# Performance work log

Measured on AMD Instinct MI355X. Metric: run time of the kernel, lower is better.

Reference implementation:

```python
import jax, jax.numpy as jnp
import numpy as np

N = 100000        # points
C_IN = 64         # in_planes
C_OUT = 64        # out_planes (== mid_planes)
SHARE = 8         # share_planes
NS = 16           # nsample
CW = C_OUT // SHARE  # attention channels (8)
EPS = 1e-5


def _bn(x, gamma, beta):
    # PointBatchNorm in training mode: normalize over all axes except channel (last)
    ax = tuple(range(x.ndim - 1))
    m = jnp.mean(x, axis=ax)
    v = jnp.var(x, axis=ax)
    return gamma * (x - m) * jax.lax.rsqrt(v + EPS) + beta


def setup_inputs() -> dict:
    key = jax.random.key(0)
    ks = jax.random.split(key, 20)
    s = 0.05
    inp = {
        "p": jax.random.normal(ks[0], (N, 3), jnp.float32) * 5.0,
        "x": jax.random.normal(ks[1], (N, C_IN), jnp.float32),
        "o": jnp.array([N], jnp.int32),
        "idx": jax.random.randint(ks[2], (N, NS), 0, N, jnp.int32),
        # q/k/v linears
        "Wq": jax.random.normal(ks[3], (C_IN, C_OUT), jnp.float32) * s,
        "bq": jnp.zeros((C_OUT,), jnp.float32),
        "Wk": jax.random.normal(ks[4], (C_IN, C_OUT), jnp.float32) * s,
        "bk": jnp.zeros((C_OUT,), jnp.float32),
        "Wv": jax.random.normal(ks[5], (C_IN, C_OUT), jnp.float32) * s,
        "bv": jnp.zeros((C_OUT,), jnp.float32),
        # linear_p: Linear(3,3) -> BN(3) -> ReLU -> Linear(3,out)
        "Wp1": jax.random.normal(ks[6], (3, 3), jnp.float32) * 0.5,
        "bp1": jnp.zeros((3,), jnp.float32),
        "gp": jnp.ones((3,), jnp.float32),
        "betap": jnp.zeros((3,), jnp.float32),
        "Wp2": jax.random.normal(ks[7], (3, C_OUT), jnp.float32) * s,
        "bp2": jnp.zeros((C_OUT,), jnp.float32),
        # linear_w: BN(mid)->ReLU->Linear(mid, CW)->BN(CW)->ReLU->Linear(CW, CW)
        "gw1": jnp.ones((C_OUT,), jnp.float32),
        "bw1": jnp.zeros((C_OUT,), jnp.float32),
        "Ww1": jax.random.normal(ks[8], (C_OUT, CW), jnp.float32) * s,
        "bww1": jnp.zeros((CW,), jnp.float32),
        "gw2": jnp.ones((CW,), jnp.float32),
        "bw2": jnp.zeros((CW,), jnp.float32),
        "Ww2": jax.random.normal(ks[9], (CW, CW), jnp.float32) * s,
        "bww2": jnp.zeros((CW,), jnp.float32),
    }
    return inp


def reference(p, x, o, idx,
              Wq, bq, Wk, bk, Wv, bv,
              Wp1, bp1, gp, betap, Wp2, bp2,
              gw1, bw1, Ww1, bww1, gw2, bw2, Ww2, bww2):
    relu = jax.nn.relu
    x_q = x @ Wq + bq                       # [n, mid]
    x_k = x @ Wk + bk                       # [n, mid]
    x_v = x @ Wv + bv                       # [n, out]
    # knn_query_and_group: gather neighbors (idx precomputed), with relative xyz
    p_r0 = p[idx] - p[:, None, :]           # [n, ns, 3]
    xk_g = x_k[idx]                         # [n, ns, mid]
    xv_g = x_v[idx]                         # [n, ns, out]
    # linear_p
    p_r = relu(_bn(p_r0 @ Wp1 + bp1, gp, betap)) @ Wp2 + bp2   # [n, ns, out]
    # einops.reduce 'n ns (i j) -> n ns j' with j=mid_planes: i==1 -> identity
    r_qk = xk_g - x_q[:, None, :] + p_r     # [n, ns, mid]
    # linear_w
    w = relu(_bn(r_qk, gw1, bw1)) @ Ww1 + bww1          # [n, ns, CW]
    w = relu(_bn(w, gw2, bw2)) @ Ww2 + bww2             # [n, ns, CW]
    w = jax.nn.softmax(w, axis=1)                        # softmax over neighbors
    # shared-channel weighted sum
    v = (xv_g + p_r).reshape(N, NS, SHARE, CW)           # [n, ns, s, i]
    out = jnp.einsum('ntsi,nti->nsi', v, w)              # [n, s, i]
    return out.reshape(N, C_OUT)
```

## Files before the change

kernel.cpp:

```cpp
#include <hip/hip_runtime.h>
#include <math.h>

#define NPTS 100000
#define NSAMP 16
#define NROWS (NPTS*NSAMP)
#define EPS 1e-5f

#define NQKV ((NPTS + 63)/64)
#define GRID_B 1024
#define GRID_C 2048
#define GRID_D 2048
#define GRID_E 2048

#define S_BN1A 0
#define S_BN1B 4
#define S_BN2A 8
#define S_BN2B 72
#define S_BN3A 136
#define S_BN3B 144
#define S_PARTB 160
#define S_PARTC (S_PARTB + GRID_B*8)
#define S_PARTD (S_PARTC + GRID_C*128)

typedef __attribute__((ext_vector_type(8))) _Float16 f16x8;
typedef __attribute__((ext_vector_type(4))) float f32x4;

__device__ __forceinline__ float bf2f(unsigned short u) {
    return __uint_as_float(((unsigned int)u) << 16);
}
__device__ __forceinline__ unsigned int cvt_pk_bf16(float lo, float hi) {
    unsigned int r;
    asm("v_cvt_pk_bf16_f32 %0, %1, %2" : "=v"(r) : "v"(lo), "v"(hi));
    return r;
}
__device__ __forceinline__ float rlF(float v, int t) {
    return __int_as_float(__builtin_amdgcn_readlane(__float_as_int(v), t));
}

__global__ __launch_bounds__(256) void qkv_bn1_kernel(
    const float* __restrict__ x,
    const float* __restrict__ Wq, const float* __restrict__ bq,
    const float* __restrict__ Wk, const float* __restrict__ bk,
    const float* __restrict__ Wv, const float* __restrict__ bv,
    float* __restrict__ xq, unsigned short* __restrict__ xkb,
    unsigned short* __restrict__ xvb,
    const float* __restrict__ p, const int* __restrict__ idx,
    const float* __restrict__ Wp1, const float* __restrict__ bp1,
    float* __restrict__ part)
{
    __shared__ __align__(16) float xsh[64][68];
    __shared__ __align__(16) float wsh[64][64];
    __shared__ float red16[4][6];
    const int tid = threadIdx.x;

    if (blockIdx.x >= NQKV) {
        const int b = blockIdx.x - NQKV;
        float w9[9], bb[3];
        #pragma unroll
        for (int i = 0; i < 9; ++i) w9[i] = Wp1[i];
        #pragma unroll
        for (int i = 0; i < 3; ++i) bb[i] = bp1[i];

        float s0=0.f,s1=0.f,s2=0.f,q0=0.f,q1=0.f,q2=0.f;
        for (int row = b*256 + tid; row < NROWS; row += GRID_B*256) {
            const int n = row >> 4;
            const int j = idx[row];
            const float d0 = p[j*3+0] - p[n*3+0];
            const float d1 = p[j*3+1] - p[n*3+1];
            const float d2 = p[j*3+2] - p[n*3+2];
            const float t0 = d0*w9[0] + d1*w9[3] + d2*w9[6] + bb[0];
            const float t1 = d0*w9[1] + d1*w9[4] + d2*w9[7] + bb[1];
            const float t2 = d0*w9[2] + d1*w9[5] + d2*w9[8] + bb[2];
            s0 += t0; s1 += t1; s2 += t2;
            q0 += t0*t0; q1 += t1*t1; q2 += t2*t2;
        }
        #pragma unroll
        for (int m = 32; m >= 1; m >>= 1) {
            s0 += __shfl_xor(s0, m); s1 += __shfl_xor(s1, m); s2 += __shfl_xor(s2, m);
            q0 += __shfl_xor(q0, m); q1 += __shfl_xor(q1, m); q2 += __shfl_xor(q2, m);
        }
        const int lane = tid & 63, wid = tid >> 6;
        if (lane == 0) {
            red16[wid][0]=s0; red16[wid][1]=s1; red16[wid][2]=s2;
            red16[wid][3]=q0; red16[wid][4]=q1; red16[wid][5]=q2;
        }
        __syncthreads();
        if (tid < 6)
            part[b*8 + tid] = red16[0][tid]+red16[1][tid]+red16[2][tid]+red16[3][tid];
        return;
    }

    const int r0 = blockIdx.x * 64;
    {
        const int row = tid >> 4, c4 = tid & 15;
        #pragma unroll
        for (int rr = 0; rr < 4; ++rr) {
            const int r = row + rr*16;
            const int gr = r0 + r;
            float4 v = (gr < NPTS) ? *(const float4*)&x[(size_t)gr*64 + c4*4]
                                   : make_float4(0.f, 0.f, 0.f, 0.f);
            *(float4*)&xsh[r][c4*4] = v;
        }
    }

    const int tr = tid >> 4, tc = tid & 15;

    for (int m = 0; m < 3; ++m) {
        const float* __restrict__ W  = (m == 0) ? Wq : (m == 1) ? Wk : Wv;
        const float* __restrict__ bs = (m == 0) ? bq : (m == 1) ? bk : bv;

        __syncthreads();
        for (int l = tid; l < 1024; l += 256)
            *(float4*)&wsh[l >> 4][(l & 15)*4] = *(const float4*)&W[l*4];
        __syncthreads();

        float acc[4][4];
        {
            const float4 b4 = *(const float4*)&bs[tc*4];
            #pragma unroll
            for (int rr = 0; rr < 4; ++rr) {
                acc[rr][0] = b4.x; acc[rr][1] = b4.y;
                acc[rr][2] = b4.z; acc[rr][3] = b4.w;
            }
        }

        #pragma unroll 4
        for (int k4 = 0; k4 < 16; ++k4) {
            float4 xr[4];
            #pragma unroll
            for (int rr = 0; rr < 4; ++rr)
                xr[rr] = *(const float4*)&xsh[tr + 16*rr][k4*4];
            float4 wr[4];
            #pragma unroll
            for (int kk = 0; kk < 4; ++kk)
                wr[kk] = *(const float4*)&wsh[k4*4 + kk][tc*4];
            #pragma unroll
            for (int rr = 0; rr < 4; ++rr) {
                acc[rr][0] += xr[rr].x*wr[0].x + xr[rr].y*wr[1].x + xr[rr].z*wr[2].x + xr[rr].w*wr[3].x;
                acc[rr][1] += xr[rr].x*wr[0].y + xr[rr].y*wr[1].y + xr[rr].z*wr[2].y + xr[rr].w*wr[3].y;
                acc[rr][2] += xr[rr].x*wr[0].z + xr[rr].y*wr[1].z + xr[rr].z*wr[2].z + xr[rr].w*wr[3].z;
                acc[rr][3] += xr[rr].x*wr[0].w + xr[rr].y*wr[1].w + xr[rr].z*wr[2].w + xr[rr].w*wr[3].w;
            }
        }

        #pragma unroll
        for (int rr = 0; rr < 4; ++rr) {
            const int gr = r0 + tr + 16*rr;
            if (gr < NPTS) {
                if (m == 0) {
                    float4 o;
                    o.x = acc[rr][0]; o.y = acc[rr][1]; o.z = acc[rr][2]; o.w = acc[rr][3];
                    *(float4*)&xq[(size_t)gr*64 + tc*4] = o;
                } else {
                    unsigned short* dst = (m == 1) ? xkb : xvb;
                    uint2 o;
                    o.x = cvt_pk_bf16(acc[rr][0], acc[rr][1]);
                    o.y = cvt_pk_bf16(acc[rr][2], acc[rr][3]);
                    *(uint2*)&dst[(size_t)gr*64 + tc*4] = o;
                }
            }
        }
    }
}

__global__ __launch_bounds__(256) void bn_fin_kernel(
    const float* __restrict__ part, int nblk, int stride, int nch,
    const float* __restrict__ g, const float* __restrict__ beta,
    float* __restrict__ aout, float* __restrict__ bout)
{
    const int c = blockIdx.x;
    const int tid = threadIdx.x;
    float s = 0.f, q = 0.f;
    for (int b = tid; b < nblk; b += 256) {
        s += part[(size_t)b*stride + c];
        q += part[(size_t)b*stride + nch + c];
    }
    #pragma unroll
    for (int m = 32; m >= 1; m >>= 1) { s += __shfl_xor(s, m); q += __shfl_xor(q, m); }
    __shared__ float rs[4], rq[4];
    if ((tid & 63) == 0) { rs[tid >> 6] = s; rq[tid >> 6] = q; }
    __syncthreads();
    if (tid == 0) {
        s = rs[0]+rs[1]+rs[2]+rs[3];
        q = rq[0]+rq[1]+rq[2]+rq[3];
        const float inv = 1.0f / (float)NROWS;
        const float mean = s * inv;
        const float var = fmaxf(q * inv - mean*mean, 0.f);
        const float a = g[c] * rsqrtf(var + EPS);
        aout[c] = a;
        bout[c] = beta[c] - a * mean;
    }
}

__global__ __launch_bounds__(256, 8) void bn2_stats_kernel(
    const float* __restrict__ p, const int* __restrict__ idx,
    const float* __restrict__ xq, const unsigned short* __restrict__ xkb,
    const float* __restrict__ Wp1, const float* __restrict__ bp1,
    const float* __restrict__ Wp2, const float* __restrict__ bp2,
    const float* __restrict__ st, float* __restrict__ part)
{
    const int tid = threadIdx.x, lane = tid & 63, wid = tid >> 6;
    float w9[9], bb[3], a1[3], b1[3];
    #pragma unroll
    for (int i = 0; i < 9; ++i) w9[i] = Wp1[i];
    #pragma unroll
    for (int i = 0; i < 3; ++i) { bb[i] = bp1[i]; a1[i] = st[S_BN1A+i]; b1[i] = st[S_BN1B+i]; }
    const float wc0 = Wp2[lane], wc1 = Wp2[64+lane], wc2 = Wp2[128+lane], bpc = bp2[lane];
    const int lane16 = lane & 15;

    float s = 0.f, q = 0.f;
    const int nw = gridDim.x * 4;
    for (int pt = blockIdx.x*4 + wid; pt < NPTS; pt += nw) {
        const float xqc = xq[(size_t)pt*64 + lane];
        const int jreg = idx[pt*16 + lane16];
        const float pn0 = p[pt*3], pn1 = p[pt*3+1], pn2 = p[pt*3+2];
        const float d0 = p[jreg*3] - pn0, d1 = p[jreg*3+1] - pn1, d2 = p[jreg*3+2] - pn2;
        const float t0 = d0*w9[0] + d1*w9[3] + d2*w9[6] + bb[0];
        const float t1 = d0*w9[1] + d1*w9[4] + d2*w9[7] + bb[1];
        const float t2 = d0*w9[2] + d1*w9[5] + d2*w9[8] + bb[2];
        const float h0 = fmaxf(a1[0]*t0 + b1[0], 0.f);
        const float h1 = fmaxf(a1[1]*t1 + b1[1], 0.f);
        const float h2 = fmaxf(a1[2]*t2 + b1[2], 0.f);

        #pragma unroll
        for (int t = 0; t < 16; ++t) {
            const int jt = __builtin_amdgcn_readlane(jreg, t);
            const float g0 = rlF(h0, t), g1 = rlF(h1, t), g2 = rlF(h2, t);
            const float pr = fmaf(g0, wc0, fmaf(g1, wc1, fmaf(g2, wc2, bpc)));
            const float r = bf2f(xkb[(size_t)jt*64 + lane]) - xqc + pr;
            s += r; q = fmaf(r, r, q);
        }
    }
    __shared__ float redS[4][64], redQ[4][64];
    redS[wid][lane] = s; redQ[wid][lane] = q;
    __syncthreads();
    if (tid < 64) {
        const float S = redS[0][tid]+redS[1][tid]+redS[2][tid]+redS[3][tid];
        const float Q = redQ[0][tid]+redQ[1][tid]+redQ[2][tid]+redQ[3][tid];
        part[(size_t)blockIdx.x*128 + tid] = S;
        part[(size_t)blockIdx.x*128 + 64 + tid] = Q;
    }
}

__global__ __launch_bounds__(256, 8) void w1_kernel(
    const float* __restrict__ p, const int* __restrict__ idx,
    const float* __restrict__ xq, const unsigned short* __restrict__ xkb,
    const float* __restrict__ Wp1, const float* __restrict__ bp1,
    const float* __restrict__ Wp2, const float* __restrict__ bp2,
    const float* __restrict__ Ww1, const float* __restrict__ bww1,
    const float* __restrict__ st, unsigned short* __restrict__ w1out,
    float* __restrict__ part)
{
    __shared__ __align__(16) _Float16 hl[4][16][64];
    const int tid = threadIdx.x, lane = tid & 63, wid = tid >> 6;

    float w9[9], bb[3], a1[3], b1[3];
    #pragma unroll
    for (int i = 0; i < 9; ++i) w9[i] = Wp1[i];
    #pragma unroll
    for (int i = 0; i < 3; ++i) { bb[i] = bp1[i]; a1[i] = st[S_BN1A+i]; b1[i] = st[S_BN1B+i]; }

    const int c = lane;
    const float wc0 = Wp2[c], wc1 = Wp2[64+c], wc2 = Wp2[128+c], bpc = bp2[c];
    const float a2c = st[S_BN2A + c], b2c = st[S_BN2B + c];
    const int lane16 = lane & 15;
    const int kgrp = lane >> 4;

    f16x8 aF0, aF1;
    {
        const int m = lane16;
        #pragma unroll
        for (int i = 0; i < 8; ++i) {
            const int k0 = kgrp*4 + (i & 3) + 16*(i >> 2);
            const int i0 = (m < 8) ? (k0*8 + m) : 0;
            const int i1 = (m < 8) ? ((k0 + 32)*8 + m) : 0;
            aF0[i] = (m < 8) ? (_Float16)Ww1[i0] : (_Float16)0.f;
            aF1[i] = (m < 8) ? (_Float16)Ww1[i1] : (_Float16)0.f;
        }
    }
    f32x4 cb;
    #pragma unroll
    for (int r = 0; r < 4; ++r) cb[r] = bww1[(kgrp*4 + r) & 7];

    float s3[4] = {0.f,0.f,0.f,0.f}, q3[4] = {0.f,0.f,0.f,0.f};
    const int nw = gridDim.x * 4;
    for (int pt = blockIdx.x*4 + wid; pt < NPTS; pt += nw) {
        const float xqc = xq[(size_t)pt*64 + lane];
        const int jreg = idx[pt*16 + lane16];
        const float pn0 = p[pt*3], pn1 = p[pt*3+1], pn2 = p[pt*3+2];
        const float d0 = p[jreg*3] - pn0, d1 = p[jreg*3+1] - pn1, d2 = p[jreg*3+2] - pn2;
        const float t0v = d0*w9[0] + d1*w9[3] + d2*w9[6] + bb[0];
        const float t1v = d0*w9[1] + d1*w9[4] + d2*w9[7] + bb[1];
        const float t2v = d0*w9[2] + d1*w9[5] + d2*w9[8] + bb[2];
        const float h0 = fmaxf(a1[0]*t0v + b1[0], 0.f);
        const float h1 = fmaxf(a1[1]*t1v + b1[1], 0.f);
        const float h2 = fmaxf(a1[2]*t2v + b1[2], 0.f);

        #pragma unroll
        for (int t = 0; t < 16; ++t) {
            const int jt = __builtin_amdgcn_readlane(jreg, t);
            const float g0 = rlF(h0, t), g1 = rlF(h1, t), g2 = rlF(h2, t);
            const float pr = fmaf(g0, wc0, fmaf(g1, wc1, fmaf(g2, wc2, bpc)));
            const float r = bf2f(xkb[(size_t)jt*64 + lane]) - xqc + pr;
            hl[wid][t][lane ^ ((t & 7) << 3)] = (_Float16)fmaxf(fmaf(a2c, r, b2c), 0.f);
        }

        const int t = lane16;
        const int key = (t & 7) << 3;
        union { f16x8 v; uint2 u[2]; } b0u, b1u;
        b0u.u[0] = *(const uint2*)&hl[wid][t][(kgrp*4)      ^ key];
        b0u.u[1] = *(const uint2*)&hl[wid][t][(kgrp*4 + 16) ^ key];
        b1u.u[0] = *(const uint2*)&hl[wid][t][(kgrp*4 + 32) ^ key];
        b1u.u[1] = *(const uint2*)&hl[wid][t][(kgrp*4 + 48) ^ key];

        f32x4 acc = __builtin_amdgcn_mfma_f32_16x16x32_f16(aF0, b0u.v, cb, 0, 0, 0);
        acc = __builtin_amdgcn_mfma_f32_16x16x32_f16(aF1, b1u.v, acc, 0, 0, 0);

        if (lane < 32) {
            uint2 o;
            o.x = cvt_pk_bf16(acc[0], acc[1]);
            o.y = cvt_pk_bf16(acc[2], acc[3]);
            *(uint2*)&w1out[(size_t)pt*128 + lane16*8 + kgrp*4] = o;
            #pragma unroll
            for (int r = 0; r < 4; ++r) {
                s3[r] += acc[r];
                q3[r] = fmaf(acc[r], acc[r], q3[r]);
            }
        }
    }

    #pragma unroll
    for (int m = 8; m >= 1; m >>= 1) {
        #pragma unroll
        for (int r = 0; r < 4; ++r) {
            s3[r] += __shfl_xor(s3[r], m);
            q3[r] += __shfl_xor(q3[r], m);
        }
    }
    __shared__ float redS[4][8], redQ[4][8];
    if (lane == 0 || lane == 16) {
        const int jb = (lane >> 4) * 4;
        #pragma unroll
        for (int r = 0; r < 4; ++r) { redS[wid][jb+r] = s3[r]; redQ[wid][jb+r] = q3[r]; }
    }
    __syncthreads();
    if (tid < 8) {
        const float S = redS[0][tid]+redS[1][tid]+redS[2][tid]+redS[3][tid];
        const float Q = redQ[0][tid]+redQ[1][tid]+redQ[2][tid]+redQ[3][tid];
        part[(size_t)blockIdx.x*16 + tid]     = S;
        part[(size_t)blockIdx.x*16 + 8 + tid] = Q;
    }
}

__global__ __launch_bounds__(256, 8) void out_kernel(
    const float* __restrict__ p, const int* __restrict__ idx,
    const unsigned short* __restrict__ xvb, const unsigned short* __restrict__ w1b,
    const float* __restrict__ Wp1, const float* __restrict__ bp1,
    const float* __restrict__ Wp2, const float* __restrict__ bp2,
    const float* __restrict__ Ww2, const float* __restrict__ bww2,
    const float* __restrict__ st, float* __restrict__ out)
{
    __shared__ float wl[4][16][8];
    const int tid = threadIdx.x, lane = tid & 63, wid = tid >> 6;
    const int j8 = lane & 7, t0 = lane >> 3;
    const int lane16 = lane & 15;

    float w9[9], bb[3], a1[3], b1[3];
    #pragma unroll
    for (int i = 0; i < 9; ++i) w9[i] = Wp1[i];
    #pragma unroll
    for (int i = 0; i < 3; ++i) { bb[i] = bp1[i]; a1[i] = st[S_BN1A+i]; b1[i] = st[S_BN1B+i]; }
    float ww2c[8];
    #pragma unroll
    for (int i = 0; i < 8; ++i) ww2c[i] = Ww2[i*8 + j8];
    const float a3j = st[S_BN3A + j8], b3j = st[S_BN3B + j8];
    const float bw2j = bww2[j8];
    const int c = lane;
    const float wc0 = Wp2[c], wc1 = Wp2[64+c], wc2 = Wp2[128+c], bpc = bp2[c];

    const int nw = gridDim.x * 4;
    for (int pt = blockIdx.x*4 + wid; pt < NPTS; pt += nw) {
        const int jreg = idx[pt*16 + lane16];
        const float pn0 = p[pt*3], pn1 = p[pt*3+1], pn2 = p[pt*3+2];
        const float d0 = p[jreg*3] - pn0, d1 = p[jreg*3+1] - pn1, d2 = p[jreg*3+2] - pn2;
        const float t1v = d0*w9[0] + d1*w9[3] + d2*w9[6] + bb[0];
        const float t2v = d0*w9[1] + d1*w9[4] + d2*w9[7] + bb[1];
        const float t3v = d0*w9[2] + d1*w9[5] + d2*w9[8] + bb[2];
        const float h0 = fmaxf(a1[0]*t1v + b1[0], 0.f);
        const float h1 = fmaxf(a1[1]*t2v + b1[1], 0.f);
        const float h2 = fmaxf(a1[2]*t3v + b1[2], 0.f);

        const float val0 = bf2f(w1b[(size_t)pt*128 + lane]);
        const float val1 = bf2f(w1b[(size_t)pt*128 + 64 + lane]);
        const float r0 = fmaxf(a3j*val0 + b3j, 0.f);
        const float r1 = fmaxf(a3j*val1 + b3j, 0.f);
        float v0 = bw2j, v1 = bw2j;
        const int gbase = lane & 56;
        #pragma unroll
        for (int jj = 0; jj < 8; ++jj) {
            v0 += __shfl(r0, gbase + jj) * ww2c[jj];
            v1 += __shfl(r1, gbase + jj) * ww2c[jj];
        }
        float e0 = __expf(v0), e1 = __expf(v1);
        float ssum = e0 + e1;
        ssum += __shfl_xor(ssum, 8);
        ssum += __shfl_xor(ssum, 16);
        ssum += __shfl_xor(ssum, 32);
        const float inv = 1.0f / ssum;
        wl[wid][t0][j8]     = e0 * inv;
        wl[wid][t0 + 8][j8] = e1 * inv;

        float acc = 0.f;
        #pragma unroll
        for (int t = 0; t < 16; ++t) {
            const int jt = __builtin_amdgcn_readlane(jreg, t);
            const float g0 = rlF(h0, t), g1 = rlF(h1, t), g2 = rlF(h2, t);
            const float pr = fmaf(g0, wc0, fmaf(g1, wc1, fmaf(g2, wc2, bpc)));
            const float wt = wl[wid][t][j8];
            acc = fmaf(bf2f(xvb[(size_t)jt*64 + c]) + pr, wt, acc);
        }
        out[(size_t)pt*64 + c] = acc;
    }
}

extern "C" void kernel_launch(void* const* d_in, const int* in_sizes, int n_in,
                              void* d_out, int out_size, void* d_ws, size_t ws_size,
                              hipStream_t stream)
{
    const float* p    = (const float*)d_in[0];
    const float* x    = (const float*)d_in[1];
    const int*   idx  = (const int*)d_in[3];
    const float* Wq   = (const float*)d_in[4];
    const float* bq   = (const float*)d_in[5];
    const float* Wk   = (const float*)d_in[6];
    const float* bk   = (const float*)d_in[7];
    const float* Wv   = (const float*)d_in[8];
    const float* bv   = (const float*)d_in[9];
    const float* Wp1  = (const float*)d_in[10];
    const float* bp1  = (const float*)d_in[11];
    const float* gp   = (const float*)d_in[12];
    const float* betap= (const float*)d_in[13];
    const float* Wp2  = (const float*)d_in[14];
    const float* bp2  = (const float*)d_in[15];
    const float* gw1  = (const float*)d_in[16];
    const float* bw1  = (const float*)d_in[17];
    const float* Ww1  = (const float*)d_in[18];
    const float* bww1 = (const float*)d_in[19];
    const float* gw2  = (const float*)d_in[20];
    const float* bw2  = (const float*)d_in[21];
    const float* Ww2  = (const float*)d_in[22];
    const float* bww2 = (const float*)d_in[23];

    float* out = (float*)d_out;
    float* ws  = (float*)d_ws;

    float*          xq  = ws;
    unsigned short* xkb = (unsigned short*)(ws + (size_t)NPTS*64);
    unsigned short* xvb = (unsigned short*)(ws + (size_t)NPTS*96);
    unsigned short* w1b = (unsigned short*)(ws + (size_t)NPTS*128);
    float*          st  = ws + (size_t)NPTS*192;

    qkv_bn1_kernel<<<NQKV + GRID_B, 256, 0, stream>>>(
        x, Wq, bq, Wk, bk, Wv, bv, xq, xkb, xvb,
        p, idx, Wp1, bp1, st + S_PARTB);
    bn_fin_kernel<<<3, 256, 0, stream>>>(st + S_PARTB, GRID_B, 8, 3, gp, betap,
                                         st + S_BN1A, st + S_BN1B);

    bn2_stats_kernel<<<GRID_C, 256, 0, stream>>>(p, idx, xq, xkb, Wp1, bp1, Wp2, bp2,
                                                 st, st + S_PARTC);
    bn_fin_kernel<<<64, 256, 0, stream>>>(st + S_PARTC, GRID_C, 128, 64, gw1, bw1,
                                          st + S_BN2A, st + S_BN2B);

    w1_kernel<<<GRID_D, 256, 0, stream>>>(p, idx, xq, xkb, Wp1, bp1, Wp2, bp2,
                                          Ww1, bww1, st, w1b, st + S_PARTD);
    bn_fin_kernel<<<8, 256, 0, stream>>>(st + S_PARTD, GRID_D, 16, 8, gw2, bw2,
                                         st + S_BN3A, st + S_BN3B);

    out_kernel<<<GRID_E, 256, 0, stream>>>(p, idx, xvb, w1b, Wp1, bp1, Wp2, bp2,
                                           Ww2, bww2, st, out);
}
```

Measured before the change: 252.8 us.

## Cache linear_p first-layer outputs in bf16 and store xq as bf16

The first pass now writes the pre-BN linear_p outputs (t0..t2) per neighbor row as packed bf16. The three later kernels read these instead of re-gathering p at random neighbor indices and recomputing the 3x3 linear. xq is also stored in bf16 rather than fp32, halving its traffic. This trades three random gathers of p per row for one coalesced 8-byte load, at the cost of an extra 12.8 MB write and bf16 rounding of both xq and the pre-BN positional features.

```diff
diff --git a/kernel.cpp b/kernel.cpp
--- a/kernel.cpp
+++ b/kernel.cpp
@@ -42,11 +42,11 @@
     const float* __restrict__ Wq, const float* __restrict__ bq,
     const float* __restrict__ Wk, const float* __restrict__ bk,
     const float* __restrict__ Wv, const float* __restrict__ bv,
-    float* __restrict__ xq, unsigned short* __restrict__ xkb,
+    unsigned short* __restrict__ xqb, unsigned short* __restrict__ xkb,
     unsigned short* __restrict__ xvb,
     const float* __restrict__ p, const int* __restrict__ idx,
     const float* __restrict__ Wp1, const float* __restrict__ bp1,
-    float* __restrict__ part)
+    unsigned short* __restrict__ tb, float* __restrict__ part)
 {
     __shared__ __align__(16) float xsh[64][68];
     __shared__ __align__(16) float wsh[64][64];
@@ -71,6 +71,10 @@
             const float t0 = d0*w9[0] + d1*w9[3] + d2*w9[6] + bb[0];
             const float t1 = d0*w9[1] + d1*w9[4] + d2*w9[7] + bb[1];
             const float t2 = d0*w9[2] + d1*w9[5] + d2*w9[8] + bb[2];
+            uint2 o;
+            o.x = cvt_pk_bf16(t0, t1);
+            o.y = cvt_pk_bf16(t2, 0.f);
+            *(uint2*)&tb[(size_t)row*4] = o;
             s0 += t0; s1 += t1; s2 += t2;
             q0 += t0*t0; q1 += t1*t1; q2 += t2*t2;
         }
@@ -108,6 +112,7 @@
     for (int m = 0; m < 3; ++m) {
         const float* __restrict__ W  = (m == 0) ? Wq : (m == 1) ? Wk : Wv;
         const float* __restrict__ bs = (m == 0) ? bq : (m == 1) ? bk : bv;
+        unsigned short* __restrict__ dst = (m == 0) ? xqb : (m == 1) ? xkb : xvb;
 
         __syncthreads();
         for (int l = tid; l < 1024; l += 256)
@@ -147,17 +152,10 @@
         for (int rr = 0; rr < 4; ++rr) {
             const int gr = r0 + tr + 16*rr;
             if (gr < NPTS) {
-                if (m == 0) {
-                    float4 o;
-                    o.x = acc[rr][0]; o.y = acc[rr][1]; o.z = acc[rr][2]; o.w = acc[rr][3];
-                    *(float4*)&xq[(size_t)gr*64 + tc*4] = o;
-                } else {
-                    unsigned short* dst = (m == 1) ? xkb : xvb;
-                    uint2 o;
-                    o.x = cvt_pk_bf16(acc[rr][0], acc[rr][1]);
-                    o.y = cvt_pk_bf16(acc[rr][2], acc[rr][3]);
-                    *(uint2*)&dst[(size_t)gr*64 + tc*4] = o;
-                }
+                uint2 o;
+                o.x = cvt_pk_bf16(acc[rr][0], acc[rr][1]);
+                o.y = cvt_pk_bf16(acc[rr][2], acc[rr][3]);
+                *(uint2*)&dst[(size_t)gr*64 + tc*4] = o;
             }
         }
     }
@@ -193,31 +191,27 @@
 }
 
 __global__ __launch_bounds__(256, 8) void bn2_stats_kernel(
-    const float* __restrict__ p, const int* __restrict__ idx,
-    const float* __restrict__ xq, const unsigned short* __restrict__ xkb,
-    const float* __restrict__ Wp1, const float* __restrict__ bp1,
+    const int* __restrict__ idx, const unsigned short* __restrict__ tb,
+    const unsigned short* __restrict__ xqb, const unsigned short* __restrict__ xkb,
     const float* __restrict__ Wp2, const float* __restrict__ bp2,
     const float* __restrict__ st, float* __restrict__ part)
 {
     const int tid = threadIdx.x, lane = tid & 63, wid = tid >> 6;
-    float w9[9], bb[3], a1[3], b1[3];
-    #pragma unroll
-    for (int i = 0; i < 9; ++i) w9[i] = Wp1[i];
-    #pragma unroll
-    for (int i = 0; i < 3; ++i) { bb[i] = bp1[i]; a1[i] = st[S_BN1A+i]; b1[i] = st[S_BN1B+i]; }
+    float a1[3], b1[3];
+    #pragma unroll
+    for (int i = 0; i < 3; ++i) { a1[i] = st[S_BN1A+i]; b1[i] = st[S_BN1B+i]; }
     const float wc0 = Wp2[lane], wc1 = Wp2[64+lane], wc2 = Wp2[128+lane], bpc = bp2[lane];
     const int lane16 = lane & 15;
 
     float s = 0.f, q = 0.f;
     const int nw = gridDim.x * 4;
     for (int pt = blockIdx.x*4 + wid; pt < NPTS; pt += nw) {
-        const float xqc = xq[(size_t)pt*64 + lane];
+        const float xqc = bf2f(xqb[(size_t)pt*64 + lane]);
         const int jreg = idx[pt*16 + lane16];
-        const float pn0 = p[pt*3], pn1 = p[pt*3+1], pn2 = p[pt*3+2];
-        const float d0 = p[jreg*3] - pn0, d1 = p[jreg*3+1] - pn1, d2 = p[jreg*3+2] - pn2;
-        const float t0 = d0*w9[0] + d1*w9[3] + d2*w9[6] + bb[0];
-        const float t1 = d0*w9[1] + d1*w9[4] + d2*w9[7] + bb[1];
-        const float t2 = d0*w9[2] + d1*w9[5] + d2*w9[8] + bb[2];
+        const uint2 tv = *(const uint2*)&tb[(size_t)(pt*16 + lane16)*4];
+        const float t0 = bf2f((unsigned short)tv.x);
+        const float t1 = bf2f((unsigned short)(tv.x >> 16));
+        const float t2 = bf2f((unsigned short)tv.y);
         const float h0 = fmaxf(a1[0]*t0 + b1[0], 0.f);
         const float h1 = fmaxf(a1[1]*t1 + b1[1], 0.f);
         const float h2 = fmaxf(a1[2]*t2 + b1[2], 0.f);
@@ -243,9 +237,8 @@
 }
 
 __global__ __launch_bounds__(256, 8) void w1_kernel(
-    const float* __restrict__ p, const int* __restrict__ idx,
-    const float* __restrict__ xq, const unsigned short* __restrict__ xkb,
-    const float* __restrict__ Wp1, const float* __restrict__ bp1,
+    const int* __restrict__ idx, const unsigned short* __restrict__ tb,
+    const unsigned short* __restrict__ xqb, const unsigned short* __restrict__ xkb,
     const float* __restrict__ Wp2, const float* __restrict__ bp2,
     const float* __restrict__ Ww1, const float* __restrict__ bww1,
     const float* __restrict__ st, unsigned short* __restrict__ w1out,
@@ -254,11 +247,9 @@
     __shared__ __align__(16) _Float16 hl[4][16][64];
     const int tid = threadIdx.x, lane = tid & 63, wid = tid >> 6;
 
-    float w9[9], bb[3], a1[3], b1[3];
-    #pragma unroll
-    for (int i = 0; i < 9; ++i) w9[i] = Wp1[i];
-    #pragma unroll
-    for (int i = 0; i < 3; ++i) { bb[i] = bp1[i]; a1[i] = st[S_BN1A+i]; b1[i] = st[S_BN1B+i]; }
+    float a1[3], b1[3];
+    #pragma unroll
+    for (int i = 0; i < 3; ++i) { a1[i] = st[S_BN1A+i]; b1[i] = st[S_BN1B+i]; }
 
     const int c = lane;
     const float wc0 = Wp2[c], wc1 = Wp2[64+c], wc2 = Wp2[128+c], bpc = bp2[c];
@@ -285,13 +276,12 @@
     float s3[4] = {0.f,0.f,0.f,0.f}, q3[4] = {0.f,0.f,0.f,0.f};
     const int nw = gridDim.x * 4;
     for (int pt = blockIdx.x*4 + wid; pt < NPTS; pt += nw) {
-        const float xqc = xq[(size_t)pt*64 + lane];
+        const float xqc = bf2f(xqb[(size_t)pt*64 + lane]);
         const int jreg = idx[pt*16 + lane16];
-        const float pn0 = p[pt*3], pn1 = p[pt*3+1], pn2 = p[pt*3+2];
-        const float d0 = p[jreg*3] - pn0, d1 = p[jreg*3+1] - pn1, d2 = p[jreg*3+2] - pn2;
-        const float t0v = d0*w9[0] + d1*w9[3] + d2*w9[6] + bb[0];
-        const float t1v = d0*w9[1] + d1*w9[4] + d2*w9[7] + bb[1];
-        const float t2v = d0*w9[2] + d1*w9[5] + d2*w9[8] + bb[2];
+        const uint2 tv = *(const uint2*)&tb[(size_t)(pt*16 + lane16)*4];
+        const float t0v = bf2f((unsigned short)tv.x);
+        const float t1v = bf2f((unsigned short)(tv.x >> 16));
+        const float t2v = bf2f((unsigned short)tv.y);
         const float h0 = fmaxf(a1[0]*t0v + b1[0], 0.f);
         const float h1 = fmaxf(a1[1]*t1v + b1[1], 0.f);
         const float h2 = fmaxf(a1[2]*t2v + b1[2], 0.f);
@@ -353,9 +343,8 @@
 }
 
 __global__ __launch_bounds__(256, 8) void out_kernel(
-    const float* __restrict__ p, const int* __restrict__ idx,
+    const int* __restrict__ idx, const unsigned short* __restrict__ tb,
     const unsigned short* __restrict__ xvb, const unsigned short* __restrict__ w1b,
-    const float* __restrict__ Wp1, const float* __restrict__ bp1,
     const float* __restrict__ Wp2, const float* __restrict__ bp2,
     const float* __restrict__ Ww2, const float* __restrict__ bww2,
     const float* __restrict__ st, float* __restrict__ out)
@@ -365,11 +354,9 @@
     const int j8 = lane & 7, t0 = lane >> 3;
     const int lane16 = lane & 15;
 
-    float w9[9], bb[3], a1[3], b1[3];
-    #pragma unroll
-    for (int i = 0; i < 9; ++i) w9[i] = Wp1[i];
-    #pragma unroll
-    for (int i = 0; i < 3; ++i) { bb[i] = bp1[i]; a1[i] = st[S_BN1A+i]; b1[i] = st[S_BN1B+i]; }
+    float a1[3], b1[3];
+    #pragma unroll
+    for (int i = 0; i < 3; ++i) { a1[i] = st[S_BN1A+i]; b1[i] = st[S_BN1B+i]; }
     float ww2c[8];
     #pragma unroll
     for (int i = 0; i < 8; ++i) ww2c[i] = Ww2[i*8 + j8];
@@ -381,11 +368,10 @@
     const int nw = gridDim.x * 4;
     for (int pt = blockIdx.x*4 + wid; pt < NPTS; pt += nw) {
         const int jreg = idx[pt*16 + lane16];
-        const float pn0 = p[pt*3], pn1 = p[pt*3+1], pn2 = p[pt*3+2];
-        const float d0 = p[jreg*3] - pn0, d1 = p[jreg*3+1] - pn1, d2 = p[jreg*3+2] - pn2;
-        const float t1v = d0*w9[0] + d1*w9[3] + d2*w9[6] + bb[0];
-        const float t2v = d0*w9[1] + d1*w9[4] + d2*w9[7] + bb[1];
-        const float t3v = d0*w9[2] + d1*w9[5] + d2*w9[8] + bb[2];
+        const uint2 tv = *(const uint2*)&tb[(size_t)(pt*16 + lane16)*4];
+        const float t1v = bf2f((unsigned short)tv.x);
+        const float t2v = bf2f((unsigned short)(tv.x >> 16));
+        const float t3v = bf2f((unsigned short)tv.y);
         const float h0 = fmaxf(a1[0]*t1v + b1[0], 0.f);
         const float h1 = fmaxf(a1[1]*t2v + b1[1], 0.f);
         const float h2 = fmaxf(a1[2]*t3v + b1[2], 0.f);
@@ -454,28 +440,29 @@
     float* out = (float*)d_out;
     float* ws  = (float*)d_ws;
 
-    float*          xq  = ws;
-    unsigned short* xkb = (unsigned short*)(ws + (size_t)NPTS*64);
-    unsigned short* xvb = (unsigned short*)(ws + (size_t)NPTS*96);
-    unsigned short* w1b = (unsigned short*)(ws + (size_t)NPTS*128);
+    unsigned short* xqb = (unsigned short*)ws;
+    unsigned short* xkb = (unsigned short*)(ws + (size_t)NPTS*32);
+    unsigned short* xvb = (unsigned short*)(ws + (size_t)NPTS*64);
+    unsigned short* w1b = (unsigned short*)(ws + (size_t)NPTS*96);
+    unsigned short* tb  = (unsigned short*)(ws + (size_t)NPTS*160);
     float*          st  = ws + (size_t)NPTS*192;
 
     qkv_bn1_kernel<<<NQKV + GRID_B, 256, 0, stream>>>(
-        x, Wq, bq, Wk, bk, Wv, bv, xq, xkb, xvb,
-        p, idx, Wp1, bp1, st + S_PARTB);
+        x, Wq, bq, Wk, bk, Wv, bv, xqb, xkb, xvb,
+        p, idx, Wp1, bp1, tb, st + S_PARTB);
     bn_fin_kernel<<<3, 256, 0, stream>>>(st + S_PARTB, GRID_B, 8, 3, gp, betap,
                                          st + S_BN1A, st + S_BN1B);
 
-    bn2_stats_kernel<<<GRID_C, 256, 0, stream>>>(p, idx, xq, xkb, Wp1, bp1, Wp2, bp2,
+    bn2_stats_kernel<<<GRID_C, 256, 0, stream>>>(idx, tb, xqb, xkb, Wp2, bp2,
                                                  st, st + S_PARTC);
     bn_fin_kernel<<<64, 256, 0, stream>>>(st + S_PARTC, GRID_C, 128, 64, gw1, bw1,
                                           st + S_BN2A, st + S_BN2B);
 
-    w1_kernel<<<GRID_D, 256, 0, stream>>>(p, idx, xq, xkb, Wp1, bp1, Wp2, bp2,
+    w1_kernel<<<GRID_D, 256, 0, stream>>>(idx, tb, xqb, xkb, Wp2, bp2,
                                           Ww1, bww1, st, w1b, st + S_PARTD);
     bn_fin_kernel<<<8, 256, 0, stream>>>(st + S_PARTD, GRID_D, 16, 8, gw2, bw2,
                                          st + S_BN3A, st + S_BN3B);
 
-    out_kernel<<<GRID_E, 256, 0, stream>>>(p, idx, xvb, w1b, Wp1, bp1, Wp2, bp2,
+    out_kernel<<<GRID_E, 256, 0, stream>>>(idx, tb, xvb, w1b, Wp2, bp2,
                                            Ww2, bww2, st, out);
 }
```

After: 228.2 us. 1.11x faster.
